# Performance work log

Measured on AMD Instinct MI355X. Metric: run time of the kernel, lower is better.

## Reference

```python
import jax, jax.numpy as jnp
import numpy as np

N_NODES = 50000
N_EDGES = 800000
IN_SIZE = 128
HIDDEN = 128   # out_size * 2
OUT_SIZE = 64


def setup_inputs() -> dict:
    key = jax.random.key(0)
    ks = jax.random.split(key, 6)
    h = jax.random.normal(ks[0], (N_NODES, IN_SIZE), dtype=jnp.float32)
    W1 = jax.random.normal(ks[1], (IN_SIZE, HIDDEN), dtype=jnp.float32) * (1.0 / np.sqrt(IN_SIZE))
    b1 = jnp.zeros((HIDDEN,), dtype=jnp.float32)
    W2 = jax.random.normal(ks[2], (HIDDEN, OUT_SIZE), dtype=jnp.float32) * (1.0 / np.sqrt(HIDDEN))
    b2 = jnp.zeros((OUT_SIZE,), dtype=jnp.float32)
    src = jax.random.randint(ks[3], (N_EDGES,), 0, N_NODES, dtype=jnp.int64)
    dst = jax.random.randint(ks[4], (N_EDGES,), 0, N_NODES, dtype=jnp.int64)
    return {"h": h, "W1": W1, "b1": b1, "W2": W2, "b2": b2, "src": src, "dst": dst}


def _norms(src, dst, n_nodes):
    # DGL GraphConv norm='both': scale by out_degree^{-1/2} (src side)
    # and in_degree^{-1/2} (dst side); zero degrees clamped to 1.
    ones = jnp.ones(src.shape, dtype=jnp.float32)
    out_deg = jnp.maximum(jax.ops.segment_sum(ones, src, num_segments=n_nodes), 1.0)
    in_deg = jnp.maximum(jax.ops.segment_sum(ones, dst, num_segments=n_nodes), 1.0)
    return (out_deg ** -0.5)[:, None], (in_deg ** -0.5)[:, None]


def _graph_conv(x, W, b, src, dst, norm_out, norm_in, n_nodes):
    # h' = D_in^{-1/2} A D_out^{-1/2} x W + b
    x = x * norm_out                                   # [N, F]
    agg = jax.ops.segment_sum(x[src], dst, num_segments=n_nodes)  # SpMM: [N, F]
    return (agg * norm_in) @ W + b


def reference(h, W1, b1, W2, b2, src, dst):
    n_nodes = h.shape[0]
    norm_out, norm_in = _norms(src, dst, n_nodes)
    h = jax.nn.relu(_graph_conv(h, W1, b1, src, dst, norm_out, norm_in, n_nodes))
    h = jax.nn.relu(_graph_conv(h, W2, b2, src, dst, norm_out, norm_in, n_nodes))
    return h
```

## Files before the change

### kernel.cpp

```cpp
#include <hip/hip_runtime.h>

#define N_NODES 50000
#define N_EDGES 800000
#define IN_SIZE 128
#define HIDDEN 128
#define OUT_SIZE 64

#define CHUNKS 128
#define CHUNK_EDGES 6250
#define NBS 196
#define GA_BLOCKS 391

typedef __attribute__((ext_vector_type(8))) short bf16x8;
typedef __attribute__((ext_vector_type(4))) float f32x4;

static __device__ inline unsigned short bf16_rne(float x) {
    unsigned ua = __float_as_uint(x);
    return (unsigned short)((ua + 0x7fffu + ((ua >> 16) & 1u)) >> 16);
}

static __device__ inline unsigned pack_bf16x2(float a, float b) {
    unsigned ua = __float_as_uint(a);
    unsigned ub = __float_as_uint(b);
    unsigned ra = (ua + 0x7fffu + ((ua >> 16) & 1u)) >> 16;
    unsigned rb = (ub + 0x7fffu + ((ub >> 16) & 1u)) & 0xffff0000u;
    return ra | rb;
}

static __device__ inline unsigned pack_f16x2(float a, float b) {
    _Float16 ha = (_Float16)a, hb = (_Float16)b;
    unsigned short ua = __builtin_bit_cast(unsigned short, ha);
    unsigned short ub = __builtin_bit_cast(unsigned short, hb);
    return (unsigned)ua | ((unsigned)ub << 16);
}

static __device__ inline float2 unpack_f16x2(unsigned u) {
    _Float16 lo = __builtin_bit_cast(_Float16, (unsigned short)(u & 0xffffu));
    _Float16 hi = __builtin_bit_cast(_Float16, (unsigned short)(u >> 16));
    return make_float2((float)lo, (float)hi);
}

__global__ __launch_bounds__(256) void wpack_kernel(const float* __restrict__ W1,
                                                    unsigned short* __restrict__ wf_hi,
                                                    unsigned short* __restrict__ wf_lo) {
    int idx = blockIdx.x * 256 + threadIdx.x;
    if (idx >= 2048) return;
    int l  = idx & 63;
    int ct = (idx >> 6) & 7;
    int ks = idx >> 9;
    int col = ct * 16 + (l & 15);
    int k0  = ks * 32 + (l >> 4) * 8;
    unsigned short hi[8], lo[8];
    #pragma unroll
    for (int j = 0; j < 8; ++j) {
        float x = W1[(size_t)(k0 + j) * 128 + col];
        unsigned short h16 = bf16_rne(x);
        float fh = __uint_as_float((unsigned)h16 << 16);
        hi[j] = h16;
        lo[j] = bf16_rne(x - fh);
    }
    ((uint4*)wf_hi)[idx] = *(const uint4*)hi;
    ((uint4*)wf_lo)[idx] = *(const uint4*)lo;
}

__global__ __launch_bounds__(256) void gemmA_kernel(const float* __restrict__ h,
                                                    const unsigned short* __restrict__ wf_hi,
                                                    const unsigned short* __restrict__ wf_lo,
                                                    unsigned short* __restrict__ t1) {
    const int t  = threadIdx.x;
    const int wv = t >> 6;
    const int l  = t & 63;
    const int lrow = l & 15;
    const int g    = l >> 4;
    const int n0 = blockIdx.x * 128 + wv * 32;

    int r0 = n0 + lrow;      if (r0 > N_NODES - 1) r0 = N_NODES - 1;
    int r1 = n0 + 16 + lrow; if (r1 > N_NODES - 1) r1 = N_NODES - 1;
    const float* h0 = h + (size_t)r0 * 128 + g * 8;
    const float* h1 = h + (size_t)r1 * 128 + g * 8;

    f32x4 acc[2][8];
    #pragma unroll
    for (int rt = 0; rt < 2; ++rt)
        #pragma unroll
        for (int ct = 0; ct < 8; ++ct)
            acc[rt][ct] = (f32x4){0.f, 0.f, 0.f, 0.f};

    const bf16x8* bh_base = (const bf16x8*)wf_hi;
    const bf16x8* bl_base = (const bf16x8*)wf_lo;

    for (int ks = 0; ks < 4; ++ks) {
        float a0[8], a1[8];
        *(float4*)(a0)     = *(const float4*)(h0 + ks * 32);
        *(float4*)(a0 + 4) = *(const float4*)(h0 + ks * 32 + 4);
        *(float4*)(a1)     = *(const float4*)(h1 + ks * 32);
        *(float4*)(a1 + 4) = *(const float4*)(h1 + ks * 32 + 4);

        bf16x8 a0h, a0l, a1h, a1l;
        #pragma unroll
        for (int j = 0; j < 8; ++j) {
            unsigned short hh = bf16_rne(a0[j]);
            a0h[j] = (short)hh;
            a0l[j] = (short)bf16_rne(a0[j] - __uint_as_float((unsigned)hh << 16));
            unsigned short h2 = bf16_rne(a1[j]);
            a1h[j] = (short)h2;
            a1l[j] = (short)bf16_rne(a1[j] - __uint_as_float((unsigned)h2 << 16));
        }

        #pragma unroll
        for (int ct = 0; ct < 8; ++ct) {
            const int fi = (ks * 8 + ct) * 64 + l;
            bf16x8 bh = bh_base[fi];
            bf16x8 bl = bl_base[fi];
            acc[0][ct] = __builtin_amdgcn_mfma_f32_16x16x32_bf16(a0l, bh, acc[0][ct], 0, 0, 0);
            acc[0][ct] = __builtin_amdgcn_mfma_f32_16x16x32_bf16(a0h, bl, acc[0][ct], 0, 0, 0);
            acc[0][ct] = __builtin_amdgcn_mfma_f32_16x16x32_bf16(a0h, bh, acc[0][ct], 0, 0, 0);
            acc[1][ct] = __builtin_amdgcn_mfma_f32_16x16x32_bf16(a1l, bh, acc[1][ct], 0, 0, 0);
            acc[1][ct] = __builtin_amdgcn_mfma_f32_16x16x32_bf16(a1h, bl, acc[1][ct], 0, 0, 0);
            acc[1][ct] = __builtin_amdgcn_mfma_f32_16x16x32_bf16(a1h, bh, acc[1][ct], 0, 0, 0);
        }
    }

    #pragma unroll
    for (int rt = 0; rt < 2; ++rt) {
        #pragma unroll
        for (int ct = 0; ct < 8; ++ct) {
            #pragma unroll
            for (int r = 0; r < 4; ++r) {
                int row = n0 + rt * 16 + g * 4 + r;
                if (row < N_NODES)
                    t1[(size_t)row * 128 + ct * 16 + lrow] = bf16_rne(acc[rt][ct][r]);
            }
        }
    }
}

__global__ __launch_bounds__(1024) void hist_kernel(const int* __restrict__ src,
                                                    const int* __restrict__ dst,
                                                    unsigned char* __restrict__ cntD,
                                                    unsigned char* __restrict__ cntS,
                                                    unsigned char* __restrict__ rp) {
    __shared__ unsigned hD[12500];
    __shared__ unsigned hS[12500];
    const int t = threadIdx.x;
    const int c = blockIdx.x;

    for (int i = t; i < 12500; i += 1024) { hD[i] = 0u; hS[i] = 0u; }
    __syncthreads();

    const int base = c * CHUNK_EDGES;
    for (int i = t; i < CHUNK_EDGES; i += 1024) {
        int e = base + i;
        int d = dst[e];
        int s = src[e];
        unsigned shd = (unsigned)(d & 3) * 8u;
        unsigned old = atomicAdd(&hD[d >> 2], 1u << shd);
        rp[e] = (unsigned char)((old >> shd) & 0xffu);
        atomicAdd(&hS[s >> 2], 1u << ((unsigned)(s & 3) * 8u));
    }
    __syncthreads();

    unsigned* gD = (unsigned*)cntD + (size_t)c * 12500;
    unsigned* gS = (unsigned*)cntS + (size_t)c * 12500;
    for (int i = t; i < 12500; i += 1024) { gD[i] = hD[i]; gS[i] = hS[i]; }
}

__global__ __launch_bounds__(256) void deg_scan_kernel(unsigned char* __restrict__ cntD,
                                                       const unsigned char* __restrict__ cntS,
                                                       int* __restrict__ row_ptr,
                                                       int* __restrict__ bsum,
                                                       float* __restrict__ norm_out,
                                                       float* __restrict__ norm_in) {
    const int t = threadIdx.x, lane = t & 63, w = t >> 6;
    const int n = blockIdx.x * 256 + t;
    unsigned sumD = 0u, sumS = 0u;
    if (n < N_NODES) {
        #pragma unroll 4
        for (int c = 0; c < CHUNKS; ++c) {
            size_t idx = (size_t)c * 50000 + n;
            unsigned v = cntD[idx];
            cntD[idx] = (unsigned char)sumD;
            sumD += v;
            sumS += cntS[idx];
        }
        norm_in[n]  = rsqrtf((float)(sumD ? sumD : 1u));
        norm_out[n] = rsqrtf((float)(sumS ? sumS : 1u));
    }
    __shared__ int wsum[4];
    int v = (n < N_NODES) ? (int)sumD : 0;
    int incl = v;
    #pragma unroll
    for (int d = 1; d < 64; d <<= 1) {
        int u = __shfl_up(incl, d, 64);
        if (lane >= d) incl += u;
    }
    if (lane == 63) wsum[w] = incl;
    __syncthreads();
    int woff = 0, total = 0;
    #pragma unroll
    for (int j = 0; j < 4; ++j) {
        int s = wsum[j];
        if (j < w) woff += s;
        total += s;
    }
    if (n < N_NODES) row_ptr[n] = woff + incl - v;
    if (t == 0) bsum[blockIdx.x] = total;
}

__global__ __launch_bounds__(64) void scan2_kernel(int* __restrict__ bsum,
                                                   int* __restrict__ row_ptr) {
    const int lane = threadIdx.x;
    int carry = 0;
    for (int base = 0; base < NBS; base += 64) {
        int t = base + lane;
        int v = (t < NBS) ? bsum[t] : 0;
        int incl = v;
        #pragma unroll
        for (int d = 1; d < 64; d <<= 1) {
            int u = __shfl_up(incl, d, 64);
            if (lane >= d) incl += u;
        }
        int excl = carry + incl - v;
        if (t < NBS) bsum[t] = excl;
        if (t == NBS - 1) row_ptr[N_NODES] = N_EDGES - excl;
        carry += __shfl(incl, 63, 64);
    }
}

__global__ __launch_bounds__(256) void place_kernel(const int* __restrict__ src,
                                                    const int* __restrict__ dst,
                                                    const int* __restrict__ row_ptr,
                                                    const int* __restrict__ bsum,
                                                    const unsigned char* __restrict__ cntD,
                                                    const unsigned char* __restrict__ rp,
                                                    int* __restrict__ eidx) {
    int e = blockIdx.x * 256 + threadIdx.x;
    if (e < N_EDGES) {
        int d = dst[e];
        int c = e / CHUNK_EDGES;
        int pos = row_ptr[d] + bsum[d >> 8] + (int)cntD[(size_t)c * 50000 + d] + (int)rp[e];
        eidx[pos] = src[e];
    }
}

__global__ __launch_bounds__(256) void gemmB_kernel(const float* __restrict__ h1p,
                                                    const float* __restrict__ W2,
                                                    unsigned short* __restrict__ t2h) {
    __shared__ float sA[32][128];
    __shared__ float sW[128][64];
    const int t  = threadIdx.x;
    const int tx = t & 15;
    const int ty = t >> 4;
    const int n0 = blockIdx.x * 32;

    for (int i = t; i < 1024; i += 256) {
        int n = i >> 5, c = i & 31;
        int gn = n0 + n;
        float4 v = make_float4(0.f, 0.f, 0.f, 0.f);
        if (gn < N_NODES) v = ((const float4*)(h1p + (size_t)gn * 128))[c];
        ((float4*)sA[n])[c] = v;
    }
    for (int i = t; i < 2048; i += 256) {
        int k = i >> 4, c = i & 15;
        ((float4*)sW[k])[c] = ((const float4*)(W2 + (size_t)k * 64))[c];
    }
    __syncthreads();

    float4 a0 = make_float4(0.f, 0.f, 0.f, 0.f);
    float4 a1 = make_float4(0.f, 0.f, 0.f, 0.f);
    #pragma unroll 4
    for (int k4 = 0; k4 < 128; k4 += 4) {
        float x0[4], x1[4];
        *(float4*)x0 = *(const float4*)&sA[ty * 2 + 0][k4];
        *(float4*)x1 = *(const float4*)&sA[ty * 2 + 1][k4];
        #pragma unroll
        for (int kk = 0; kk < 4; ++kk) {
            float4 w = ((float4*)sW[k4 + kk])[tx];
            a0.x = fmaf(x0[kk], w.x, a0.x); a0.y = fmaf(x0[kk], w.y, a0.y);
            a0.z = fmaf(x0[kk], w.z, a0.z); a0.w = fmaf(x0[kk], w.w, a0.w);
            a1.x = fmaf(x1[kk], w.x, a1.x); a1.y = fmaf(x1[kk], w.y, a1.y);
            a1.z = fmaf(x1[kk], w.z, a1.z); a1.w = fmaf(x1[kk], w.w, a1.w);
        }
    }

    #pragma unroll
    for (int ni = 0; ni < 2; ++ni) {
        int gn = n0 + ty * 2 + ni;
        if (gn < N_NODES) {
            float4 a = ni ? a1 : a0;
            uint2 p;
            p.x = pack_f16x2(a.x, a.y);
            p.y = pack_f16x2(a.z, a.w);
            ((uint2*)(t2h + (size_t)gn * 64))[tx] = p;
        }
    }
}

__global__ __launch_bounds__(256) void pull128_kernel(const unsigned short* __restrict__ xb,
                                                      const int* __restrict__ row_ptr,
                                                      const int* __restrict__ bsum,
                                                      const int* __restrict__ eidx,
                                                      const float* __restrict__ b1,
                                                      const float* __restrict__ norm_in,
                                                      const float* __restrict__ norm_out,
                                                      float* __restrict__ out) {
    int node = blockIdx.x * 4 + (threadIdx.x >> 6);
    node = __builtin_amdgcn_readfirstlane(node);
    const int lane = threadIdx.x & 63;
    const int beg = __builtin_amdgcn_readfirstlane(row_ptr[node] + bsum[node >> 8]);
    const int end = __builtin_amdgcn_readfirstlane(row_ptr[node + 1] + bsum[(node + 1) >> 8]);

    float2 acc0 = make_float2(0.f, 0.f);
    float2 acc1 = make_float2(0.f, 0.f);
    float2 acc2 = make_float2(0.f, 0.f);
    float2 acc3 = make_float2(0.f, 0.f);

    for (int base = beg; base < end; base += 64) {
        const int cnt = min(64, end - base);
        int my_e = 0;
        float my_n = 0.f;
        if (lane < cnt) {
            my_e = eidx[base + lane];
            my_n = norm_out[my_e];
        }
        int k = 0;
        for (; k + 7 < cnt; k += 8) {
            int s0 = __builtin_amdgcn_readlane(my_e, k);
            int s1 = __builtin_amdgcn_readlane(my_e, k + 1);
            int s2 = __builtin_amdgcn_readlane(my_e, k + 2);
            int s3 = __builtin_amdgcn_readlane(my_e, k + 3);
            int s4 = __builtin_amdgcn_readlane(my_e, k + 4);
            int s5 = __builtin_amdgcn_readlane(my_e, k + 5);
            int s6 = __builtin_amdgcn_readlane(my_e, k + 6);
            int s7 = __builtin_amdgcn_readlane(my_e, k + 7);
            float n0 = __int_as_float(__builtin_amdgcn_readlane(__float_as_int(my_n), k));
            float n1 = __int_as_float(__builtin_amdgcn_readlane(__float_as_int(my_n), k + 1));
            float n2 = __int_as_float(__builtin_amdgcn_readlane(__float_as_int(my_n), k + 2));
            float n3 = __int_as_float(__builtin_amdgcn_readlane(__float_as_int(my_n), k + 3));
            float n4 = __int_as_float(__builtin_amdgcn_readlane(__float_as_int(my_n), k + 4));
            float n5 = __int_as_float(__builtin_amdgcn_readlane(__float_as_int(my_n), k + 5));
            float n6 = __int_as_float(__builtin_amdgcn_readlane(__float_as_int(my_n), k + 6));
            float n7 = __int_as_float(__builtin_amdgcn_readlane(__float_as_int(my_n), k + 7));
            unsigned u0 = ((const unsigned*)(xb + (size_t)s0 * 128))[lane];
            unsigned u1 = ((const unsigned*)(xb + (size_t)s1 * 128))[lane];
            unsigned u2 = ((const unsigned*)(xb + (size_t)s2 * 128))[lane];
            unsigned u3 = ((const unsigned*)(xb + (size_t)s3 * 128))[lane];
            unsigned u4 = ((const unsigned*)(xb + (size_t)s4 * 128))[lane];
            unsigned u5 = ((const unsigned*)(xb + (size_t)s5 * 128))[lane];
            unsigned u6 = ((const unsigned*)(xb + (size_t)s6 * 128))[lane];
            unsigned u7 = ((const unsigned*)(xb + (size_t)s7 * 128))[lane];
            acc0.x = fmaf(__uint_as_float(u0 << 16), n0, acc0.x);
            acc0.y = fmaf(__uint_as_float(u0 & 0xffff0000u), n0, acc0.y);
            acc1.x = fmaf(__uint_as_float(u1 << 16), n1, acc1.x);
            acc1.y = fmaf(__uint_as_float(u1 & 0xffff0000u), n1, acc1.y);
            acc2.x = fmaf(__uint_as_float(u2 << 16), n2, acc2.x);
            acc2.y = fmaf(__uint_as_float(u2 & 0xffff0000u), n2, acc2.y);
            acc3.x = fmaf(__uint_as_float(u3 << 16), n3, acc3.x);
            acc3.y = fmaf(__uint_as_float(u3 & 0xffff0000u), n3, acc3.y);
            acc0.x = fmaf(__uint_as_float(u4 << 16), n4, acc0.x);
            acc0.y = fmaf(__uint_as_float(u4 & 0xffff0000u), n4, acc0.y);
            acc1.x = fmaf(__uint_as_float(u5 << 16), n5, acc1.x);
            acc1.y = fmaf(__uint_as_float(u5 & 0xffff0000u), n5, acc1.y);
            acc2.x = fmaf(__uint_as_float(u6 << 16), n6, acc2.x);
            acc2.y = fmaf(__uint_as_float(u6 & 0xffff0000u), n6, acc2.y);
            acc3.x = fmaf(__uint_as_float(u7 << 16), n7, acc3.x);
            acc3.y = fmaf(__uint_as_float(u7 & 0xffff0000u), n7, acc3.y);
        }
        for (; k + 3 < cnt; k += 4) {
            int s0 = __builtin_amdgcn_readlane(my_e, k);
            int s1 = __builtin_amdgcn_readlane(my_e, k + 1);
            int s2 = __builtin_amdgcn_readlane(my_e, k + 2);
            int s3 = __builtin_amdgcn_readlane(my_e, k + 3);
            float n0 = __int_as_float(__builtin_amdgcn_readlane(__float_as_int(my_n), k));
            float n1 = __int_as_float(__builtin_amdgcn_readlane(__float_as_int(my_n), k + 1));
            float n2 = __int_as_float(__builtin_amdgcn_readlane(__float_as_int(my_n), k + 2));
            float n3 = __int_as_float(__builtin_amdgcn_readlane(__float_as_int(my_n), k + 3));
            unsigned u0 = ((const unsigned*)(xb + (size_t)s0 * 128))[lane];
            unsigned u1 = ((const unsigned*)(xb + (size_t)s1 * 128))[lane];
            unsigned u2 = ((const unsigned*)(xb + (size_t)s2 * 128))[lane];
            unsigned u3 = ((const unsigned*)(xb + (size_t)s3 * 128))[lane];
            acc0.x = fmaf(__uint_as_float(u0 << 16), n0, acc0.x);
            acc0.y = fmaf(__uint_as_float(u0 & 0xffff0000u), n0, acc0.y);
            acc1.x = fmaf(__uint_as_float(u1 << 16), n1, acc1.x);
            acc1.y = fmaf(__uint_as_float(u1 & 0xffff0000u), n1, acc1.y);
            acc2.x = fmaf(__uint_as_float(u2 << 16), n2, acc2.x);
            acc2.y = fmaf(__uint_as_float(u2 & 0xffff0000u), n2, acc2.y);
            acc3.x = fmaf(__uint_as_float(u3 << 16), n3, acc3.x);
            acc3.y = fmaf(__uint_as_float(u3 & 0xffff0000u), n3, acc3.y);
        }
        for (; k < cnt; ++k) {
            int s0 = __builtin_amdgcn_readlane(my_e, k);
            float n0 = __int_as_float(__builtin_amdgcn_readlane(__float_as_int(my_n), k));
            unsigned u0 = ((const unsigned*)(xb + (size_t)s0 * 128))[lane];
            acc0.x = fmaf(__uint_as_float(u0 << 16), n0, acc0.x);
            acc0.y = fmaf(__uint_as_float(u0 & 0xffff0000u), n0, acc0.y);
        }
    }

    float ni = norm_in[node];
    float no = norm_out[node];
    float2 bb = ((const float2*)b1)[lane];
    float sx = (acc0.x + acc1.x) + (acc2.x + acc3.x);
    float sy = (acc0.y + acc1.y) + (acc2.y + acc3.y);
    float2 r;
    r.x = fmaxf(fmaf(sx, ni, bb.x), 0.f) * no;
    r.y = fmaxf(fmaf(sy, ni, bb.y), 0.f) * no;
    ((float2*)(out + (size_t)node * 128))[lane] = r;
}

__global__ __launch_bounds__(256) void pull64_kernel(const unsigned* __restrict__ x,
                                                     const int* __restrict__ row_ptr,
                                                     const int* __restrict__ bsum,
                                                     const int* __restrict__ eidx,
                                                     const float* __restrict__ b2,
                                                     const float* __restrict__ norm_in,
                                                     float* __restrict__ out) {
    int node = blockIdx.x * 4 + (threadIdx.x >> 6);
    node = __builtin_amdgcn_readfirstlane(node);
    const int lane = threadIdx.x & 63;
    const int half = lane >> 5;
    const int fl = lane & 31;
    const int beg = __builtin_amdgcn_readfirstlane(row_ptr[node] + bsum[node >> 8]);
    const int end = __builtin_amdgcn_readfirstlane(row_ptr[node + 1] + bsum[(node + 1) >> 8]);

    float2 a0 = make_float2(0.f, 0.f);
    float2 a1 = make_float2(0.f, 0.f);
    float2 a2 = make_float2(0.f, 0.f);
    float2 a3 = make_float2(0.f, 0.f);

    for (int base = beg; base < end; base += 64) {
        const int cnt = min(64, end - base);
        int my_e = (lane < cnt) ? eidx[base + lane] : 0;
        int k = 0;
        for (; k + 7 < cnt; k += 8) {
            int sa0 = __builtin_amdgcn_readlane(my_e, k);
            int sb0 = __builtin_amdgcn_readlane(my_e, k + 1);
            int sa1 = __builtin_amdgcn_readlane(my_e, k + 2);
            int sb1 = __builtin_amdgcn_readlane(my_e, k + 3);
            int sa2 = __builtin_amdgcn_readlane(my_e, k + 4);
            int sb2 = __builtin_amdgcn_readlane(my_e, k + 5);
            int sa3 = __builtin_amdgcn_readlane(my_e, k + 6);
            int sb3 = __builtin_amdgcn_readlane(my_e, k + 7);
            int e0 = half ? sb0 : sa0;
            int e1 = half ? sb1 : sa1;
            int e2 = half ? sb2 : sa2;
            int e3 = half ? sb3 : sa3;
            unsigned u0 = x[(size_t)e0 * 32 + fl];
            unsigned u1 = x[(size_t)e1 * 32 + fl];
            unsigned u2 = x[(size_t)e2 * 32 + fl];
            unsigned u3 = x[(size_t)e3 * 32 + fl];
            float2 v0 = unpack_f16x2(u0);
            float2 v1 = unpack_f16x2(u1);
            float2 v2 = unpack_f16x2(u2);
            float2 v3 = unpack_f16x2(u3);
            a0.x += v0.x; a0.y += v0.y;
            a1.x += v1.x; a1.y += v1.y;
            a2.x += v2.x; a2.y += v2.y;
            a3.x += v3.x; a3.y += v3.y;
        }
        for (; k + 1 < cnt; k += 2) {
            int sa = __builtin_amdgcn_readlane(my_e, k);
            int sb = __builtin_amdgcn_readlane(my_e, k + 1);
            int e0 = half ? sb : sa;
            unsigned u = x[(size_t)e0 * 32 + fl];
            float2 v = unpack_f16x2(u);
            a0.x += v.x; a0.y += v.y;
        }
        if (k < cnt) {
            int sa = __builtin_amdgcn_readlane(my_e, k);
            if (half == 0) {
                unsigned u = x[(size_t)sa * 32 + fl];
                float2 v = unpack_f16x2(u);
                a0.x += v.x; a0.y += v.y;
            }
        }
    }

    float ax = (a0.x + a1.x) + (a2.x + a3.x);
    float ay = (a0.y + a1.y) + (a2.y + a3.y);
    ax += __shfl_xor(ax, 32, 64);
    ay += __shfl_xor(ay, 32, 64);
    if (half == 0) {
        float ni = norm_in[node];
        float2 bb = ((const float2*)b2)[fl];
        float2 r;
        r.x = fmaxf(fmaf(ax, ni, bb.x), 0.f);
        r.y = fmaxf(fmaf(ay, ni, bb.y), 0.f);
        ((float2*)(out + (size_t)node * 64))[fl] = r;
    }
}

extern "C" void kernel_launch(void* const* d_in, const int* in_sizes, int n_in,
                              void* d_out, int out_size, void* d_ws, size_t ws_size,
                              hipStream_t stream) {
    const float* h  = (const float*)d_in[0];
    const float* W1 = (const float*)d_in[1];
    const float* b1 = (const float*)d_in[2];
    const float* W2 = (const float*)d_in[3];
    const float* b2 = (const float*)d_in[4];
    const int* src  = (const int*)d_in[5];
    const int* dst  = (const int*)d_in[6];
    float* out = (float*)d_out;

    char* ws = (char*)d_ws;
    size_t off = 0;
    auto alloc = [&](size_t bytes) {
        void* p = ws + off;
        off = (off + bytes + 255) & ~(size_t)255;
        return p;
    };
    float* norm_out   = (float*)alloc(N_NODES * sizeof(float));
    float* norm_in    = (float*)alloc(N_NODES * sizeof(float));
    int* row_ptr      = (int*)alloc((N_NODES + 1) * sizeof(int));
    int* bsum         = (int*)alloc(NBS * sizeof(int));
    unsigned short* wf_hi = (unsigned short*)alloc(2048 * 16);
    unsigned short* wf_lo = (unsigned short*)alloc(2048 * 16);
    int* eidx         = (int*)alloc((size_t)N_EDGES * sizeof(int));
    unsigned short* t1 = (unsigned short*)alloc((size_t)N_NODES * 128 * sizeof(short));
    float* h1p        = (float*)alloc((size_t)N_NODES * 128 * sizeof(float));

    unsigned char* cntD = (unsigned char*)h1p;
    unsigned char* cntS = cntD + (size_t)CHUNKS * 50000;
    unsigned char* rp   = cntS + (size_t)CHUNKS * 50000;
    unsigned short* t2h = t1;

    wpack_kernel<<<8, 256, 0, stream>>>(W1, wf_hi, wf_lo);

    hist_kernel<<<CHUNKS, 1024, 0, stream>>>(src, dst, cntD, cntS, rp);

    gemmA_kernel<<<GA_BLOCKS, 256, 0, stream>>>(h, wf_hi, wf_lo, t1);

    deg_scan_kernel<<<NBS, 256, 0, stream>>>(cntD, cntS, row_ptr, bsum, norm_out, norm_in);

    scan2_kernel<<<1, 64, 0, stream>>>(bsum, row_ptr);

    place_kernel<<<(N_EDGES + 255) / 256, 256, 0, stream>>>(src, dst, row_ptr, bsum, cntD, rp, eidx);

    pull128_kernel<<<N_NODES / 4, 256, 0, stream>>>(t1, row_ptr, bsum, eidx, b1,
                                                    norm_in, norm_out, h1p);

    gemmB_kernel<<<(N_NODES + 31) / 32, 256, 0, stream>>>(h1p, W2, t2h);
    pull64_kernel<<<N_NODES / 4, 256, 0, stream>>>((const unsigned*)t2h, row_ptr, bsum, eidx,
                                                   b2, norm_in, out);
}
```

Before: 214.6 us.

## Use split-bf16 MFMA for second GEMM and fold norm_out into first GEMM epilogue

Replaces the FP32 LDS-tiled second GEMM with a split-bf16 (hi/lo) MFMA kernel, and pre-packs W2 in the weight-pack kernel. Applies the source-side norm_out scaling in the first GEMM's epilogue, so the 128-wide pull kernel no longer gathers a per-edge norm or broadcasts it with readlane and just adds the gathered values. gemmA is moved after the degree scan so norm_out is ready when it runs. Together these are meant to cut the second GEMM's FP32 FMA and LDS cost and the extra work in the first aggregation, at the price of the three-pass split-bf16 approximation and a GEMM that now waits on the graph-setup kernels.

```diff
diff --git a/kernel.cpp b/kernel.cpp
--- a/kernel.cpp
+++ b/kernel.cpp
@@ -19,19 +19,13 @@
     return (unsigned short)((ua + 0x7fffu + ((ua >> 16) & 1u)) >> 16);
 }
 
-static __device__ inline unsigned pack_bf16x2(float a, float b) {
-    unsigned ua = __float_as_uint(a);
-    unsigned ub = __float_as_uint(b);
-    unsigned ra = (ua + 0x7fffu + ((ua >> 16) & 1u)) >> 16;
-    unsigned rb = (ub + 0x7fffu + ((ub >> 16) & 1u)) & 0xffff0000u;
-    return ra | rb;
+static __device__ inline unsigned short f16_bits(float x) {
+    _Float16 hx = (_Float16)x;
+    return __builtin_bit_cast(unsigned short, hx);
 }
 
 static __device__ inline unsigned pack_f16x2(float a, float b) {
-    _Float16 ha = (_Float16)a, hb = (_Float16)b;
-    unsigned short ua = __builtin_bit_cast(unsigned short, ha);
-    unsigned short ub = __builtin_bit_cast(unsigned short, hb);
-    return (unsigned)ua | ((unsigned)ub << 16);
+    return (unsigned)f16_bits(a) | ((unsigned)f16_bits(b) << 16);
 }
 
 static __device__ inline float2 unpack_f16x2(unsigned u) {
@@ -41,31 +35,52 @@
 }
 
 __global__ __launch_bounds__(256) void wpack_kernel(const float* __restrict__ W1,
+                                                    const float* __restrict__ W2,
                                                     unsigned short* __restrict__ wf_hi,
-                                                    unsigned short* __restrict__ wf_lo) {
+                                                    unsigned short* __restrict__ wf_lo,
+                                                    unsigned short* __restrict__ wf2_hi,
+                                                    unsigned short* __restrict__ wf2_lo) {
     int idx = blockIdx.x * 256 + threadIdx.x;
-    if (idx >= 2048) return;
-    int l  = idx & 63;
-    int ct = (idx >> 6) & 7;
-    int ks = idx >> 9;
-    int col = ct * 16 + (l & 15);
-    int k0  = ks * 32 + (l >> 4) * 8;
-    unsigned short hi[8], lo[8];
-    #pragma unroll
-    for (int j = 0; j < 8; ++j) {
-        float x = W1[(size_t)(k0 + j) * 128 + col];
-        unsigned short h16 = bf16_rne(x);
-        float fh = __uint_as_float((unsigned)h16 << 16);
-        hi[j] = h16;
-        lo[j] = bf16_rne(x - fh);
-    }
-    ((uint4*)wf_hi)[idx] = *(const uint4*)hi;
-    ((uint4*)wf_lo)[idx] = *(const uint4*)lo;
+    if (idx < 2048) {
+        int l  = idx & 63;
+        int ct = (idx >> 6) & 7;
+        int ks = idx >> 9;
+        int col = ct * 16 + (l & 15);
+        int k0  = ks * 32 + (l >> 4) * 8;
+        unsigned short hi[8], lo[8];
+        #pragma unroll
+        for (int j = 0; j < 8; ++j) {
+            float x = W1[(size_t)(k0 + j) * 128 + col];
+            unsigned short h16 = bf16_rne(x);
+            hi[j] = h16;
+            lo[j] = bf16_rne(x - __uint_as_float((unsigned)h16 << 16));
+        }
+        ((uint4*)wf_hi)[idx] = *(const uint4*)hi;
+        ((uint4*)wf_lo)[idx] = *(const uint4*)lo;
+    } else if (idx < 3072) {
+        int i2 = idx - 2048;
+        int l  = i2 & 63;
+        int ct = (i2 >> 6) & 3;
+        int ks = i2 >> 8;
+        int col = ct * 16 + (l & 15);
+        int k0  = ks * 32 + (l >> 4) * 8;
+        unsigned short hi[8], lo[8];
+        #pragma unroll
+        for (int j = 0; j < 8; ++j) {
+            float x = W2[(size_t)(k0 + j) * 64 + col];
+            unsigned short h16 = bf16_rne(x);
+            hi[j] = h16;
+            lo[j] = bf16_rne(x - __uint_as_float((unsigned)h16 << 16));
+        }
+        ((uint4*)wf2_hi)[i2] = *(const uint4*)hi;
+        ((uint4*)wf2_lo)[i2] = *(const uint4*)lo;
+    }
 }
 
 __global__ __launch_bounds__(256) void gemmA_kernel(const float* __restrict__ h,
                                                     const unsigned short* __restrict__ wf_hi,
                                                     const unsigned short* __restrict__ wf_lo,
+                                                    const float* __restrict__ norm_out,
                                                     unsigned short* __restrict__ t1) {
     const int t  = threadIdx.x;
     const int wv = t >> 6;
@@ -123,13 +138,91 @@
 
     #pragma unroll
     for (int rt = 0; rt < 2; ++rt) {
+        float no_[4];
+        #pragma unroll
+        for (int r = 0; r < 4; ++r) {
+            int row = n0 + rt * 16 + g * 4 + r;
+            no_[r] = (row < N_NODES) ? norm_out[row] : 0.f;
+        }
         #pragma unroll
         for (int ct = 0; ct < 8; ++ct) {
             #pragma unroll
             for (int r = 0; r < 4; ++r) {
                 int row = n0 + rt * 16 + g * 4 + r;
                 if (row < N_NODES)
-                    t1[(size_t)row * 128 + ct * 16 + lrow] = bf16_rne(acc[rt][ct][r]);
+                    t1[(size_t)row * 128 + ct * 16 + lrow] = bf16_rne(acc[rt][ct][r] * no_[r]);
+            }
+        }
+    }
+}
+
+__global__ __launch_bounds__(256) void gemmB_kernel(const float* __restrict__ h1p,
+                                                    const unsigned short* __restrict__ wf2_hi,
+                                                    const unsigned short* __restrict__ wf2_lo,
+                                                    unsigned short* __restrict__ t2h) {
+    const int t  = threadIdx.x;
+    const int wv = t >> 6;
+    const int l  = t & 63;
+    const int lrow = l & 15;
+    const int g    = l >> 4;
+    const int n0 = blockIdx.x * 128 + wv * 32;
+
+    int r0 = n0 + lrow;      if (r0 > N_NODES - 1) r0 = N_NODES - 1;
+    int r1 = n0 + 16 + lrow; if (r1 > N_NODES - 1) r1 = N_NODES - 1;
+    const float* h0 = h1p + (size_t)r0 * 128 + g * 8;
+    const float* h1 = h1p + (size_t)r1 * 128 + g * 8;
+
+    f32x4 acc[2][4];
+    #pragma unroll
+    for (int rt = 0; rt < 2; ++rt)
+        #pragma unroll
+        for (int ct = 0; ct < 4; ++ct)
+            acc[rt][ct] = (f32x4){0.f, 0.f, 0.f, 0.f};
+
+    const bf16x8* bh_base = (const bf16x8*)wf2_hi;
+    const bf16x8* bl_base = (const bf16x8*)wf2_lo;
+
+    for (int ks = 0; ks < 4; ++ks) {
+        float a0[8], a1[8];
+        *(float4*)(a0)     = *(const float4*)(h0 + ks * 32);
+        *(float4*)(a0 + 4) = *(const float4*)(h0 + ks * 32 + 4);
+        *(float4*)(a1)     = *(const float4*)(h1 + ks * 32);
+        *(float4*)(a1 + 4) = *(const float4*)(h1 + ks * 32 + 4);
+
+        bf16x8 a0h, a0l, a1h, a1l;
+        #pragma unroll
+        for (int j = 0; j < 8; ++j) {
+            unsigned short hh = bf16_rne(a0[j]);
+            a0h[j] = (short)hh;
+            a0l[j] = (short)bf16_rne(a0[j] - __uint_as_float((unsigned)hh << 16));
+            unsigned short h2 = bf16_rne(a1[j]);
+            a1h[j] = (short)h2;
+            a1l[j] = (short)bf16_rne(a1[j] - __uint_as_float((unsigned)h2 << 16));
+        }
+
+        #pragma unroll
+        for (int ct = 0; ct < 4; ++ct) {
+            const int fi = (ks * 4 + ct) * 64 + l;
+            bf16x8 bh = bh_base[fi];
+            bf16x8 bl = bl_base[fi];
+            acc[0][ct] = __builtin_amdgcn_mfma_f32_16x16x32_bf16(a0l, bh, acc[0][ct], 0, 0, 0);
+            acc[0][ct] = __builtin_amdgcn_mfma_f32_16x16x32_bf16(a0h, bl, acc[0][ct], 0, 0, 0);
+            acc[0][ct] = __builtin_amdgcn_mfma_f32_16x16x32_bf16(a0h, bh, acc[0][ct], 0, 0, 0);
+            acc[1][ct] = __builtin_amdgcn_mfma_f32_16x16x32_bf16(a1l, bh, acc[1][ct], 0, 0, 0);
+            acc[1][ct] = __builtin_amdgcn_mfma_f32_16x16x32_bf16(a1h, bl, acc[1][ct], 0, 0, 0);
+            acc[1][ct] = __builtin_amdgcn_mfma_f32_16x16x32_bf16(a1h, bh, acc[1][ct], 0, 0, 0);
+        }
+    }
+
+    #pragma unroll
+    for (int rt = 0; rt < 2; ++rt) {
+        #pragma unroll
+        for (int ct = 0; ct < 4; ++ct) {
+            #pragma unroll
+            for (int r = 0; r < 4; ++r) {
+                int row = n0 + rt * 16 + g * 4 + r;
+                if (row < N_NODES)
+                    t2h[(size_t)row * 64 + ct * 16 + lrow] = f16_bits(acc[rt][ct][r]);
             }
         }
     }
@@ -243,59 +336,6 @@
     }
 }
 
-__global__ __launch_bounds__(256) void gemmB_kernel(const float* __restrict__ h1p,
-                                                    const float* __restrict__ W2,
-                                                    unsigned short* __restrict__ t2h) {
-    __shared__ float sA[32][128];
-    __shared__ float sW[128][64];
-    const int t  = threadIdx.x;
-    const int tx = t & 15;
-    const int ty = t >> 4;
-    const int n0 = blockIdx.x * 32;
-
-    for (int i = t; i < 1024; i += 256) {
-        int n = i >> 5, c = i & 31;
-        int gn = n0 + n;
-        float4 v = make_float4(0.f, 0.f, 0.f, 0.f);
-        if (gn < N_NODES) v = ((const float4*)(h1p + (size_t)gn * 128))[c];
-        ((float4*)sA[n])[c] = v;
-    }
-    for (int i = t; i < 2048; i += 256) {
-        int k = i >> 4, c = i & 15;
-        ((float4*)sW[k])[c] = ((const float4*)(W2 + (size_t)k * 64))[c];
-    }
-    __syncthreads();
-
-    float4 a0 = make_float4(0.f, 0.f, 0.f, 0.f);
-    float4 a1 = make_float4(0.f, 0.f, 0.f, 0.f);
-    #pragma unroll 4
-    for (int k4 = 0; k4 < 128; k4 += 4) {
-        float x0[4], x1[4];
-        *(float4*)x0 = *(const float4*)&sA[ty * 2 + 0][k4];
-        *(float4*)x1 = *(const float4*)&sA[ty * 2 + 1][k4];
-        #pragma unroll
-        for (int kk = 0; kk < 4; ++kk) {
-            float4 w = ((float4*)sW[k4 + kk])[tx];
-            a0.x = fmaf(x0[kk], w.x, a0.x); a0.y = fmaf(x0[kk], w.y, a0.y);
-            a0.z = fmaf(x0[kk], w.z, a0.z); a0.w = fmaf(x0[kk], w.w, a0.w);
-            a1.x = fmaf(x1[kk], w.x, a1.x); a1.y = fmaf(x1[kk], w.y, a1.y);
-            a1.z = fmaf(x1[kk], w.z, a1.z); a1.w = fmaf(x1[kk], w.w, a1.w);
-        }
-    }
-
-    #pragma unroll
-    for (int ni = 0; ni < 2; ++ni) {
-        int gn = n0 + ty * 2 + ni;
-        if (gn < N_NODES) {
-            float4 a = ni ? a1 : a0;
-            uint2 p;
-            p.x = pack_f16x2(a.x, a.y);
-            p.y = pack_f16x2(a.z, a.w);
-            ((uint2*)(t2h + (size_t)gn * 64))[tx] = p;
-        }
-    }
-}
-
 __global__ __launch_bounds__(256) void pull128_kernel(const unsigned short* __restrict__ xb,
                                                       const int* __restrict__ row_ptr,
                                                       const int* __restrict__ bsum,
@@ -317,12 +357,7 @@
 
     for (int base = beg; base < end; base += 64) {
         const int cnt = min(64, end - base);
-        int my_e = 0;
-        float my_n = 0.f;
-        if (lane < cnt) {
-            my_e = eidx[base + lane];
-            my_n = norm_out[my_e];
-        }
+        int my_e = (lane < cnt) ? eidx[base + lane] : 0;
         int k = 0;
         for (; k + 7 < cnt; k += 8) {
             int s0 = __builtin_amdgcn_readlane(my_e, k);
@@ -333,14 +368,6 @@
             int s5 = __builtin_amdgcn_readlane(my_e, k + 5);
             int s6 = __builtin_amdgcn_readlane(my_e, k + 6);
             int s7 = __builtin_amdgcn_readlane(my_e, k + 7);
-            float n0 = __int_as_float(__builtin_amdgcn_readlane(__float_as_int(my_n), k));
-            float n1 = __int_as_float(__builtin_amdgcn_readlane(__float_as_int(my_n), k + 1));
-            float n2 = __int_as_float(__builtin_amdgcn_readlane(__float_as_int(my_n), k + 2));
-            float n3 = __int_as_float(__builtin_amdgcn_readlane(__float_as_int(my_n), k + 3));
-            float n4 = __int_as_float(__builtin_amdgcn_readlane(__float_as_int(my_n), k + 4));
-            float n5 = __int_as_float(__builtin_amdgcn_readlane(__float_as_int(my_n), k + 5));
-            float n6 = __int_as_float(__builtin_amdgcn_readlane(__float_as_int(my_n), k + 6));
-            float n7 = __int_as_float(__builtin_amdgcn_readlane(__float_as_int(my_n), k + 7));
             unsigned u0 = ((const unsigned*)(xb + (size_t)s0 * 128))[lane];
             unsigned u1 = ((const unsigned*)(xb + (size_t)s1 * 128))[lane];
             unsigned u2 = ((const unsigned*)(xb + (size_t)s2 * 128))[lane];
@@ -349,51 +376,46 @@
             unsigned u5 = ((const unsigned*)(xb + (size_t)s5 * 128))[lane];
             unsigned u6 = ((const unsigned*)(xb + (size_t)s6 * 128))[lane];
             unsigned u7 = ((const unsigned*)(xb + (size_t)s7 * 128))[lane];
-            acc0.x = fmaf(__uint_as_float(u0 << 16), n0, acc0.x);
-            acc0.y = fmaf(__uint_as_float(u0 & 0xffff0000u), n0, acc0.y);
-            acc1.x = fmaf(__uint_as_float(u1 << 16), n1, acc1.x);
-            acc1.y = fmaf(__uint_as_float(u1 & 0xffff0000u), n1, acc1.y);
-            acc2.x = fmaf(__uint_as_float(u2 << 16), n2, acc2.x);
-            acc2.y = fmaf(__uint_as_float(u2 & 0xffff0000u), n2, acc2.y);
-            acc3.x = fmaf(__uint_as_float(u3 << 16), n3, acc3.x);
-            acc3.y = fmaf(__uint_as_float(u3 & 0xffff0000u), n3, acc3.y);
-            acc0.x = fmaf(__uint_as_float(u4 << 16), n4, acc0.x);
-            acc0.y = fmaf(__uint_as_float(u4 & 0xffff0000u), n4, acc0.y);
-            acc1.x = fmaf(__uint_as_float(u5 << 16), n5, acc1.x);
-            acc1.y = fmaf(__uint_as_float(u5 & 0xffff0000u), n5, acc1.y);
-            acc2.x = fmaf(__uint_as_float(u6 << 16), n6, acc2.x);
-            acc2.y = fmaf(__uint_as_float(u6 & 0xffff0000u), n6, acc2.y);
-            acc3.x = fmaf(__uint_as_float(u7 << 16), n7, acc3.x);
-            acc3.y = fmaf(__uint_as_float(u7 & 0xffff0000u), n7, acc3.y);
+            acc0.x += __uint_as_float(u0 << 16);
+            acc0.y += __uint_as_float(u0 & 0xffff0000u);
+            acc1.x += __uint_as_float(u1 << 16);
+            acc1.y += __uint_as_float(u1 & 0xffff0000u);
+            acc2.x += __uint_as_float(u2 << 16);
+            acc2.y += __uint_as_float(u2 & 0xffff0000u);
+            acc3.x += __uint_as_float(u3 << 16);
+            acc3.y += __uint_as_float(u3 & 0xffff0000u);
+            acc0.x += __uint_as_float(u4 << 16);
+            acc0.y += __uint_as_float(u4 & 0xffff0000u);
+            acc1.x += __uint_as_float(u5 << 16);
+            acc1.y += __uint_as_float(u5 & 0xffff0000u);
+            acc2.x += __uint_as_float(u6 << 16);
+            acc2.y += __uint_as_float(u6 & 0xffff0000u);
+            acc3.x += __uint_as_float(u7 << 16);
+            acc3.y += __uint_as_float(u7 & 0xffff0000u);
         }
         for (; k + 3 < cnt; k += 4) {
             int s0 = __builtin_amdgcn_readlane(my_e, k);
             int s1 = __builtin_amdgcn_readlane(my_e, k + 1);
             int s2 = __builtin_amdgcn_readlane(my_e, k + 2);
             int s3 = __builtin_amdgcn_readlane(my_e, k + 3);
-            float n0 = __int_as_float(__builtin_amdgcn_readlane(__float_as_int(my_n), k));
-            float n1 = __int_as_float(__builtin_amdgcn_readlane(__float_as_int(my_n), k + 1));
-            float n2 = __int_as_float(__builtin_amdgcn_readlane(__float_as_int(my_n), k + 2));
-            float n3 = __int_as_float(__builtin_amdgcn_readlane(__float_as_int(my_n), k + 3));
             unsigned u0 = ((const unsigned*)(xb + (size_t)s0 * 128))[lane];
             unsigned u1 = ((const unsigned*)(xb + (size_t)s1 * 128))[lane];
             unsigned u2 = ((const unsigned*)(xb + (size_t)s2 * 128))[lane];
             unsigned u3 = ((const unsigned*)(xb + (size_t)s3 * 128))[lane];
-            acc0.x = fmaf(__uint_as_float(u0 << 16), n0, acc0.x);
-            acc0.y = fmaf(__uint_as_float(u0 & 0xffff0000u), n0, acc0.y);
-            acc1.x = fmaf(__uint_as_float(u1 << 16), n1, acc1.x);
-            acc1.y = fmaf(__uint_as_float(u1 & 0xffff0000u), n1, acc1.y);
-            acc2.x = fmaf(__uint_as_float(u2 << 16), n2, acc2.x);
-            acc2.y = fmaf(__uint_as_float(u2 & 0xffff0000u), n2, acc2.y);
-            acc3.x = fmaf(__uint_as_float(u3 << 16), n3, acc3.x);
-            acc3.y = fmaf(__uint_as_float(u3 & 0xffff0000u), n3, acc3.y);
+            acc0.x += __uint_as_float(u0 << 16);
+            acc0.y += __uint_as_float(u0 & 0xffff0000u);
+            acc1.x += __uint_as_float(u1 << 16);
+            acc1.y += __uint_as_float(u1 & 0xffff0000u);
+            acc2.x += __uint_as_float(u2 << 16);
+            acc2.y += __uint_as_float(u2 & 0xffff0000u);
+            acc3.x += __uint_as_float(u3 << 16);
+            acc3.y += __uint_as_float(u3 & 0xffff0000u);
         }
         for (; k < cnt; ++k) {
             int s0 = __builtin_amdgcn_readlane(my_e, k);
-            float n0 = __int_as_float(__builtin_amdgcn_readlane(__float_as_int(my_n), k));
             unsigned u0 = ((const unsigned*)(xb + (size_t)s0 * 128))[lane];
-            acc0.x = fmaf(__uint_as_float(u0 << 16), n0, acc0.x);
-            acc0.y = fmaf(__uint_as_float(u0 & 0xffff0000u), n0, acc0.y);
+            acc0.x += __uint_as_float(u0 << 16);
+            acc0.y += __uint_as_float(u0 & 0xffff0000u);
         }
     }
 
@@ -513,8 +535,10 @@
     float* norm_in    = (float*)alloc(N_NODES * sizeof(float));
     int* row_ptr      = (int*)alloc((N_NODES + 1) * sizeof(int));
     int* bsum         = (int*)alloc(NBS * sizeof(int));
-    unsigned short* wf_hi = (unsigned short*)alloc(2048 * 16);
-    unsigned short* wf_lo = (unsigned short*)alloc(2048 * 16);
+    unsigned short* wf_hi  = (unsigned short*)alloc(2048 * 16);
+    unsigned short* wf_lo  = (unsigned short*)alloc(2048 * 16);
+    unsigned short* wf2_hi = (unsigned short*)alloc(1024 * 16);
+    unsigned short* wf2_lo = (unsigned short*)alloc(1024 * 16);
     int* eidx         = (int*)alloc((size_t)N_EDGES * sizeof(int));
     unsigned short* t1 = (unsigned short*)alloc((size_t)N_NODES * 128 * sizeof(short));
     float* h1p        = (float*)alloc((size_t)N_NODES * 128 * sizeof(float));
@@ -524,22 +548,22 @@
     unsigned char* rp   = cntS + (size_t)CHUNKS * 50000;
     unsigned short* t2h = t1;
 
-    wpack_kernel<<<8, 256, 0, stream>>>(W1, wf_hi, wf_lo);
+    wpack_kernel<<<12, 256, 0, stream>>>(W1, W2, wf_hi, wf_lo, wf2_hi, wf2_lo);
 
     hist_kernel<<<CHUNKS, 1024, 0, stream>>>(src, dst, cntD, cntS, rp);
 
-    gemmA_kernel<<<GA_BLOCKS, 256, 0, stream>>>(h, wf_hi, wf_lo, t1);
-
     deg_scan_kernel<<<NBS, 256, 0, stream>>>(cntD, cntS, row_ptr, bsum, norm_out, norm_in);
 
     scan2_kernel<<<1, 64, 0, stream>>>(bsum, row_ptr);
 
     place_kernel<<<(N_EDGES + 255) / 256, 256, 0, stream>>>(src, dst, row_ptr, bsum, cntD, rp, eidx);
+
+    gemmA_kernel<<<GA_BLOCKS, 256, 0, stream>>>(h, wf_hi, wf_lo, norm_out, t1);
 
     pull128_kernel<<<N_NODES / 4, 256, 0, stream>>>(t1, row_ptr, bsum, eidx, b1,
                                                     norm_in, norm_out, h1p);
 
-    gemmB_kernel<<<(N_NODES + 31) / 32, 256, 0, stream>>>(h1p, W2, t2h);
+    gemmB_kernel<<<GA_BLOCKS, 256, 0, stream>>>(h1p, wf2_hi, wf2_lo, t2h);
     pull64_kernel<<<N_NODES / 4, 256, 0, stream>>>((const unsigned*)t2h, row_ptr, bsum, eidx,
                                                    b2, norm_in, out);
 }
```

After: 212.0 us. Within noise of the previous version (-1.2%).
